# Kernel tuning notes

Hardware: AMD Instinct MI355X
Metric: run time of the kernel (lower is better)

Reference implementation:

```python
import jax, jax.numpy as jnp
import numpy as np

N_NODES = 10000
N_EDGES = 640000
IN_FEAT = 128
OUT_FEAT = 128


def setup_inputs() -> dict:
    key = jax.random.key(0)
    ks = jax.random.split(key, 12)
    inp = {
        "h": jax.random.normal(ks[0], (N_NODES, IN_FEAT), dtype=jnp.float32),
        "e": jax.random.uniform(ks[1], (N_EDGES, 1), dtype=jnp.float32),
        "src": jax.random.randint(ks[2], (N_EDGES,), 0, N_NODES, dtype=jnp.int32),
        "dst": jax.random.randint(ks[3], (N_EDGES,), 0, N_NODES, dtype=jnp.int32),
        # Linear params (torch convention: W [out, in], y = x @ W.T + b)
        "Ws_w": jax.random.normal(ks[4], (OUT_FEAT, IN_FEAT), dtype=jnp.float32) * 0.05,
        "Ws_b": jnp.zeros((OUT_FEAT,), dtype=jnp.float32),
        "Wn_w": jax.random.normal(ks[5], (OUT_FEAT, IN_FEAT), dtype=jnp.float32) * 0.05,
        "Wn_b": jnp.zeros((OUT_FEAT,), dtype=jnp.float32),
        "Wu_w": jax.random.normal(ks[6], (OUT_FEAT, IN_FEAT), dtype=jnp.float32) * 0.05,
        "Wu_b": jnp.zeros((OUT_FEAT,), dtype=jnp.float32),
        "lin_w": jax.random.normal(ks[7], (OUT_FEAT, OUT_FEAT), dtype=jnp.float32) * 0.05,
        "lin_b": jnp.zeros((OUT_FEAT,), dtype=jnp.float32),
    }
    return inp


def _mean_agg(msgs, dst, n_nodes):
    # segment-mean to destination nodes; isolated nodes (deg 0) -> 0 (DGL semantics)
    s = jax.ops.segment_sum(msgs, dst, num_segments=n_nodes)
    deg = jax.ops.segment_sum(jnp.ones((msgs.shape[0],), msgs.dtype), dst,
                              num_segments=n_nodes)
    return s / jnp.maximum(deg, 1.0)[:, None]


def reference(h, e, src, dst, Ws_w, Ws_b, Wn_w, Wn_b, Wu_w, Wu_b, lin_w, lin_b):
    n = h.shape[0]
    h_src = h[src]                      # [E, d] gather of source features
    h_p = _mean_agg(h_src * e, dst, n)  # u_mul_e + mean
    h_u = _mean_agg(h_src, dst, n)      # copy_u + mean
    h_total = (h @ Ws_w.T + Ws_b) + (h_p @ Wn_w.T + Wn_b) + (h_u @ Wu_w.T + Wu_b)
    return h_total @ lin_w.T + lin_b
```

## Files before the change

kernel.cpp:

```cpp
#include <hip/hip_runtime.h>
#include <hip/hip_bf16.h>

#define NFEAT 128
#define NPB 8
#define P 256
#define MAXN 10240
#define CAP 128
#define CVT 64

typedef __attribute__((ext_vector_type(8))) short bf16x8;
typedef __attribute__((ext_vector_type(4))) float f32x4;

__device__ __forceinline__ unsigned short f2bf(float f) {
    const unsigned int u = __float_as_uint(f);
    return (unsigned short)((u + 0x7FFFu + ((u >> 16) & 1u)) >> 16);
}
__device__ __forceinline__ float bflo(unsigned int u) {
    return __uint_as_float(u << 16);
}
__device__ __forceinline__ float bfhi(unsigned int u) {
    return __uint_as_float(u & 0xFFFF0000u);
}

__global__ __launch_bounds__(256) void hist_weights(
        const int* __restrict__ dst, unsigned char* __restrict__ hist,
        int n_edges, int n_nodes,
        const float* __restrict__ h, unsigned short* __restrict__ hb,
        const float* __restrict__ Ws, const float* __restrict__ Wn,
        const float* __restrict__ Wu,
        const float* __restrict__ Wsb, const float* __restrict__ Wnb,
        const float* __restrict__ Wub,
        const float* __restrict__ lin, const float* __restrict__ linb,
        unsigned short* __restrict__ Wcatb, float* __restrict__ btot) {
    __shared__ int lh[MAXN];
    __shared__ float cs[NFEAT], cn[NFEAT], cu[NFEAT], bsum[NFEAT];
    const int tid = threadIdx.x;
    if (blockIdx.x < P) {
        const int b = blockIdx.x;
        for (int n = tid; n < n_nodes; n += 256) lh[n] = 0;
        __syncthreads();
        const int per = (n_edges + P - 1) / P;
        const int beg = b * per;
        const int end = min(beg + per, n_edges);
        for (int i = beg + tid * 4; i < end; i += 1024) {
            if (i + 4 <= end) {
                const int4 d4 = *(const int4*)(dst + i);
                atomicAdd(&lh[d4.x], 1);
                atomicAdd(&lh[d4.y], 1);
                atomicAdd(&lh[d4.z], 1);
                atomicAdd(&lh[d4.w], 1);
            } else {
                for (int k = i; k < end; ++k) atomicAdd(&lh[dst[k]], 1);
            }
        }
        __syncthreads();
        unsigned char* hrow = hist + (size_t)b * n_nodes;
        const int n4 = n_nodes >> 2;
        for (int q = tid; q < n4; q += 256) {
            const int n = q * 4;
            const unsigned int v = (unsigned int)(lh[n] & 255)
                                 | ((unsigned int)(lh[n + 1] & 255) << 8)
                                 | ((unsigned int)(lh[n + 2] & 255) << 16)
                                 | ((unsigned int)(lh[n + 3] & 255) << 24);
            ((unsigned int*)hrow)[q] = v;
        }
        for (int n = n4 * 4 + tid; n < n_nodes; n += 256)
            hrow[n] = (unsigned char)lh[n];
    } else if (blockIdx.x < P + NFEAT) {
        const int i = blockIdx.x - P;
        const int o = tid;
        if (o < NFEAT) {
            cs[o] = Ws[o * NFEAT + i];
            cn[o] = Wn[o * NFEAT + i];
            cu[o] = Wu[o * NFEAT + i];
            bsum[o] = Wsb[o] + Wnb[o] + Wub[o];
        }
        __syncthreads();
        if (o < NFEAT) {
            float a1 = 0.f, a2 = 0.f, a3 = 0.f, ab = 0.f;
            #pragma unroll 4
            for (int k = 0; k < NFEAT; ++k) {
                const float l = lin[o * NFEAT + k];
                a1 += l * cs[k];
                a2 += l * cn[k];
                a3 += l * cu[k];
                ab += l * bsum[k];
            }
            const int tn = o >> 4, ncol = o & 15;
            const int kin = i & 31, quad = kin >> 3, j = kin & 7;
            const int tkbase = (i >> 5);
            const float av[3] = {a1, a2, a3};
            #pragma unroll
            for (int s = 0; s < 3; ++s) {
                const int tk = s * 4 + tkbase;
                const size_t idx =
                    ((size_t)(tk * 8 + tn) * 64 + quad * 16 + ncol) * 8 + j;
                Wcatb[idx] = f2bf(av[s]);
            }
            if (i == 0) btot[o] = ab + linb[o];
        }
    } else {
        const int b = blockIdx.x - P - NFEAT;
        const size_t total4 = (size_t)n_nodes * (NFEAT / 4);
        for (size_t q = (size_t)b * 256 + tid; q < total4; q += (size_t)CVT * 256) {
            const float4 v = *(const float4*)(h + q * 4);
            uint2 o;
            o.x = (unsigned int)f2bf(v.x) | ((unsigned int)f2bf(v.y) << 16);
            o.y = (unsigned int)f2bf(v.z) | ((unsigned int)f2bf(v.w) << 16);
            *(uint2*)(hb + q * 4) = o;
        }
    }
}

__global__ void col_scan(const unsigned char* __restrict__ hist,
                         unsigned char* __restrict__ base,
                         int* __restrict__ cnt, int n_nodes) {
    const int node = blockIdx.x * blockDim.x + threadIdx.x;
    if (node >= n_nodes) return;
    int run = 0;
    #pragma unroll 8
    for (int b = 0; b < P; ++b) {
        const int h = hist[(size_t)b * n_nodes + node];
        base[(size_t)b * n_nodes + node] = (unsigned char)run;
        run += h;
    }
    cnt[node] = run;
}

__global__ __launch_bounds__(256) void scatter_csr(
        const int* __restrict__ src, const int* __restrict__ dst,
        const float* __restrict__ e, const unsigned char* __restrict__ base,
        int2* __restrict__ eidx, int n_edges, int n_nodes) {
    __shared__ int lh[MAXN];
    const int tid = threadIdx.x;
    const int b = blockIdx.x;
    for (int n = tid; n < n_nodes; n += 256)
        lh[n] = n * CAP + (int)base[(size_t)b * n_nodes + n];
    __syncthreads();
    const int per = (n_edges + P - 1) / P;
    const int beg = b * per;
    const int end = min(beg + per, n_edges);
    for (int i = beg + tid * 4; i < end; i += 1024) {
        if (i + 4 <= end) {
            const int4 d4 = *(const int4*)(dst + i);
            const int4 s4 = *(const int4*)(src + i);
            const float4 e4 = *(const float4*)(e + i);
            int p0 = atomicAdd(&lh[d4.x], 1);
            int p1 = atomicAdd(&lh[d4.y], 1);
            int p2 = atomicAdd(&lh[d4.z], 1);
            int p3 = atomicAdd(&lh[d4.w], 1);
            if (p0 < (d4.x + 1) * CAP) eidx[p0] = make_int2(s4.x, __float_as_int(e4.x));
            if (p1 < (d4.y + 1) * CAP) eidx[p1] = make_int2(s4.y, __float_as_int(e4.y));
            if (p2 < (d4.z + 1) * CAP) eidx[p2] = make_int2(s4.z, __float_as_int(e4.z));
            if (p3 < (d4.w + 1) * CAP) eidx[p3] = make_int2(s4.w, __float_as_int(e4.w));
        } else {
            for (int k = i; k < end; ++k) {
                const int d = dst[k];
                const int pos = atomicAdd(&lh[d], 1);
                if (pos < (d + 1) * CAP)
                    eidx[pos] = make_int2(src[k], __float_as_int(e[k]));
            }
        }
    }
}

__global__ __launch_bounds__(256, 4) void agg_gemm(
        const float* __restrict__ h, const unsigned short* __restrict__ hb,
        const int2* __restrict__ eidx,
        const int* __restrict__ cnt, const unsigned short* __restrict__ Wcatb,
        const float* __restrict__ btot, float* __restrict__ out, int n_nodes) {
    __shared__ unsigned short Xsb[3][NPB][NFEAT];
    __shared__ int2 se[NPB][CAP];
    __shared__ int scnt[NPB];
    const int tid = threadIdx.x;
    const int n0 = blockIdx.x * NPB;

    if (tid < NPB) scnt[tid] = (n0 + tid < n_nodes) ? cnt[n0 + tid] : 0;
    __syncthreads();

    for (int i = tid; i < NPB * CAP; i += 256) {
        const int ln = i >> 7;
        const int k  = i & (CAP - 1);
        if (k < scnt[ln]) se[ln][k] = eidx[(size_t)(n0 + ln) * CAP + k];
    }
    {
        const int i = tid;
        const int n = i >> 5;
        const int c4 = i & 31;
        const int gn = n0 + n;
        float4 v = make_float4(0.f, 0.f, 0.f, 0.f);
        if (gn < n_nodes) v = *(const float4*)(h + (size_t)gn * NFEAT + c4 * 4);
        uint2 pk;
        pk.x = (unsigned int)f2bf(v.x) | ((unsigned int)f2bf(v.y) << 16);
        pk.y = (unsigned int)f2bf(v.z) | ((unsigned int)f2bf(v.w) << 16);
        *(uint2*)(&Xsb[0][n][c4 * 4]) = pk;
    }
    __syncthreads();

    {
        const int hw = tid >> 5;
        const int hl = tid & 31;
        const unsigned short* hbp = hb + hl * 4;
        const int ln = hw;
        const int n = scnt[ln];
        const int nl = min(n, CAP);
        float4 su = make_float4(0.f, 0.f, 0.f, 0.f);
        float4 sp = make_float4(0.f, 0.f, 0.f, 0.f);
        int j = 0;
        for (; j + 8 <= nl; j += 8) {
            int2 E[8];
            #pragma unroll
            for (int q = 0; q < 8; ++q) E[q] = se[ln][j + q];
            uint2 H[8];
            #pragma unroll
            for (int q = 0; q < 8; ++q)
                H[q] = *(const uint2*)(hbp + (size_t)E[q].x * NFEAT);
            #pragma unroll
            for (int q = 0; q < 8; ++q) {
                const float v = __int_as_float(E[q].y);
                const float h0 = bflo(H[q].x), h1 = bfhi(H[q].x);
                const float h2 = bflo(H[q].y), h3 = bfhi(H[q].y);
                su.x += h0; su.y += h1; su.z += h2; su.w += h3;
                sp.x += v * h0; sp.y += v * h1;
                sp.z += v * h2; sp.w += v * h3;
            }
        }
        for (; j < nl; ++j) {
            const int2 e0 = se[ln][j];
            const uint2 Hv = *(const uint2*)(hbp + (size_t)e0.x * NFEAT);
            const float v0 = __int_as_float(e0.y);
            const float h0 = bflo(Hv.x), h1 = bfhi(Hv.x);
            const float h2 = bflo(Hv.y), h3 = bfhi(Hv.y);
            su.x += h0; su.y += h1; su.z += h2; su.w += h3;
            sp.x += v0 * h0; sp.y += v0 * h1;
            sp.z += v0 * h2; sp.w += v0 * h3;
        }
        const float inv = 1.0f / fmaxf((float)n, 1.0f);
        uint2 pk;
        pk.x = (unsigned int)f2bf(sp.x * inv) | ((unsigned int)f2bf(sp.y * inv) << 16);
        pk.y = (unsigned int)f2bf(sp.z * inv) | ((unsigned int)f2bf(sp.w * inv) << 16);
        *(uint2*)(&Xsb[1][ln][hl * 4]) = pk;
        pk.x = (unsigned int)f2bf(su.x * inv) | ((unsigned int)f2bf(su.y * inv) << 16);
        pk.y = (unsigned int)f2bf(su.z * inv) | ((unsigned int)f2bf(su.w * inv) << 16);
        *(uint2*)(&Xsb[2][ln][hl * 4]) = pk;
    }
    __syncthreads();

    {
        const int wv   = tid >> 6;
        const int lane = tid & 63;
        const int mrow = lane & 15;
        const int quad = lane >> 4;
        const int tn0  = wv * 2;
        f32x4 acc0 = {0.f, 0.f, 0.f, 0.f};
        f32x4 acc1 = {0.f, 0.f, 0.f, 0.f};
        const bf16x8* Wb = (const bf16x8*)Wcatb;
        #pragma unroll
        for (int tk = 0; tk < 12; ++tk) {
            const int s  = tk >> 2;
            const int kb = (tk & 3) * 32 + quad * 8;
            const bf16x8 a  = *(const bf16x8*)(&Xsb[s][mrow & 7][kb]);
            const bf16x8 b0 = Wb[(size_t)(tk * 8 + tn0) * 64 + lane];
            const bf16x8 b1 = Wb[(size_t)(tk * 8 + tn0 + 1) * 64 + lane];
            acc0 = __builtin_amdgcn_mfma_f32_16x16x32_bf16(a, b0, acc0, 0, 0, 0);
            acc1 = __builtin_amdgcn_mfma_f32_16x16x32_bf16(a, b1, acc1, 0, 0, 0);
        }
        const int c0 = tn0 * 16 + mrow;
        const int c1 = (tn0 + 1) * 16 + mrow;
        const float bt0 = btot[c0];
        const float bt1 = btot[c1];
        #pragma unroll
        for (int r = 0; r < 4; ++r) {
            const int row = quad * 4 + r;
            const int gn = n0 + row;
            if (row < NPB && gn < n_nodes) {
                out[(size_t)gn * NFEAT + c0] = acc0[r] + bt0;
                out[(size_t)gn * NFEAT + c1] = acc1[r] + bt1;
            }
        }
    }
}

extern "C" void kernel_launch(void* const* d_in, const int* in_sizes, int n_in,
                              void* d_out, int out_size, void* d_ws, size_t ws_size,
                              hipStream_t stream) {
    const float* h     = (const float*)d_in[0];
    const float* e     = (const float*)d_in[1];
    const int*   src   = (const int*)d_in[2];
    const int*   dst   = (const int*)d_in[3];
    const float* Ws_w  = (const float*)d_in[4];
    const float* Ws_b  = (const float*)d_in[5];
    const float* Wn_w  = (const float*)d_in[6];
    const float* Wn_b  = (const float*)d_in[7];
    const float* Wu_w  = (const float*)d_in[8];
    const float* Wu_b  = (const float*)d_in[9];
    const float* lin_w = (const float*)d_in[10];
    const float* lin_b = (const float*)d_in[11];
    float* out = (float*)d_out;

    const int n_nodes = in_sizes[0] / NFEAT;
    const int n_edges = in_sizes[2];

    char* ws = (char*)d_ws;
    unsigned short* Wcatb = (unsigned short*)ws;  ws += 3 * NFEAT * NFEAT * 2;
    float* btot = (float*)ws;            ws += NFEAT * 4;
    int2*  eidx = (int2*)ws;             ws += (size_t)n_nodes * CAP * 8;
    int*   cnt  = (int*)ws;              ws += n_nodes * 4;
    unsigned short* hb = (unsigned short*)ws;  ws += (size_t)n_nodes * NFEAT * 2;
    unsigned char* hist = (unsigned char*)ws;  ws += (size_t)P * n_nodes;
    unsigned char* base = (unsigned char*)ws;  ws += (size_t)P * n_nodes;

    hist_weights<<<P + NFEAT + CVT, 256, 0, stream>>>(
        dst, hist, n_edges, n_nodes, h, hb,
        Ws_w, Wn_w, Wu_w, Ws_b, Wn_b, Wu_b, lin_w, lin_b, Wcatb, btot);

    col_scan<<<(n_nodes + 255) / 256, 256, 0, stream>>>(hist, base, cnt, n_nodes);

    scatter_csr<<<P, 256, 0, stream>>>(src, dst, e, base, eidx, n_edges, n_nodes);

    const int n_blocks = (n_nodes + NPB - 1) / NPB;
    agg_gemm<<<n_blocks, 256, 0, stream>>>(h, hb, eidx, cnt, Wcatb, btot,
                                           out, n_nodes);
}
```

Baseline: 137.2 us.

## Build per-node edge buckets with global atomics instead of histogram+scan+scatter

Replaces the three-pass deterministic bucket build (per-block shared histograms, column scan over 256 partial histograms, then scatter) with one pass that does a global atomicAdd on each node's counter and writes the edge into its fixed-capacity slot. Zeroing the counters moves into the weight/convert prep kernel, and the aggregation kernel now clamps the count to CAP when loading edges. This removes two kernel launches and the large byte-histogram traffic. In exchange it adds heavy global-atomic contention (about 64 edges per destination) and makes edge order within a bucket nondeterministic.

```diff
diff --git a/kernel.cpp b/kernel.cpp
--- a/kernel.cpp
+++ b/kernel.cpp
@@ -3,10 +3,9 @@
 
 #define NFEAT 128
 #define NPB 8
-#define P 256
-#define MAXN 10240
 #define CAP 128
 #define CVT 64
+#define SCB 640
 
 typedef __attribute__((ext_vector_type(8))) short bf16x8;
 typedef __attribute__((ext_vector_type(4))) float f32x4;
@@ -22,52 +21,23 @@
     return __uint_as_float(u & 0xFFFF0000u);
 }
 
-__global__ __launch_bounds__(256) void hist_weights(
-        const int* __restrict__ dst, unsigned char* __restrict__ hist,
-        int n_edges, int n_nodes,
+__global__ __launch_bounds__(256) void prep(
         const float* __restrict__ h, unsigned short* __restrict__ hb,
         const float* __restrict__ Ws, const float* __restrict__ Wn,
         const float* __restrict__ Wu,
         const float* __restrict__ Wsb, const float* __restrict__ Wnb,
         const float* __restrict__ Wub,
         const float* __restrict__ lin, const float* __restrict__ linb,
-        unsigned short* __restrict__ Wcatb, float* __restrict__ btot) {
-    __shared__ int lh[MAXN];
+        unsigned short* __restrict__ Wcatb, float* __restrict__ btot,
+        int* __restrict__ cnt, int n_nodes) {
     __shared__ float cs[NFEAT], cn[NFEAT], cu[NFEAT], bsum[NFEAT];
     const int tid = threadIdx.x;
-    if (blockIdx.x < P) {
-        const int b = blockIdx.x;
-        for (int n = tid; n < n_nodes; n += 256) lh[n] = 0;
-        __syncthreads();
-        const int per = (n_edges + P - 1) / P;
-        const int beg = b * per;
-        const int end = min(beg + per, n_edges);
-        for (int i = beg + tid * 4; i < end; i += 1024) {
-            if (i + 4 <= end) {
-                const int4 d4 = *(const int4*)(dst + i);
-                atomicAdd(&lh[d4.x], 1);
-                atomicAdd(&lh[d4.y], 1);
-                atomicAdd(&lh[d4.z], 1);
-                atomicAdd(&lh[d4.w], 1);
-            } else {
-                for (int k = i; k < end; ++k) atomicAdd(&lh[dst[k]], 1);
-            }
-        }
-        __syncthreads();
-        unsigned char* hrow = hist + (size_t)b * n_nodes;
-        const int n4 = n_nodes >> 2;
-        for (int q = tid; q < n4; q += 256) {
-            const int n = q * 4;
-            const unsigned int v = (unsigned int)(lh[n] & 255)
-                                 | ((unsigned int)(lh[n + 1] & 255) << 8)
-                                 | ((unsigned int)(lh[n + 2] & 255) << 16)
-                                 | ((unsigned int)(lh[n + 3] & 255) << 24);
-            ((unsigned int*)hrow)[q] = v;
-        }
-        for (int n = n4 * 4 + tid; n < n_nodes; n += 256)
-            hrow[n] = (unsigned char)lh[n];
-    } else if (blockIdx.x < P + NFEAT) {
-        const int i = blockIdx.x - P;
+    if (blockIdx.x < NFEAT) {
+        {
+            const int z = blockIdx.x * 256 + tid;
+            if (z < n_nodes) cnt[z] = 0;
+        }
+        const int i = blockIdx.x;
         const int o = tid;
         if (o < NFEAT) {
             cs[o] = Ws[o * NFEAT + i];
@@ -100,7 +70,7 @@
             if (i == 0) btot[o] = ab + linb[o];
         }
     } else {
-        const int b = blockIdx.x - P - NFEAT;
+        const int b = blockIdx.x - NFEAT;
         const size_t total4 = (size_t)n_nodes * (NFEAT / 4);
         for (size_t q = (size_t)b * 256 + tid; q < total4; q += (size_t)CVT * 256) {
             const float4 v = *(const float4*)(h + q * 4);
@@ -112,55 +82,29 @@
     }
 }
 
-__global__ void col_scan(const unsigned char* __restrict__ hist,
-                         unsigned char* __restrict__ base,
-                         int* __restrict__ cnt, int n_nodes) {
-    const int node = blockIdx.x * blockDim.x + threadIdx.x;
-    if (node >= n_nodes) return;
-    int run = 0;
-    #pragma unroll 8
-    for (int b = 0; b < P; ++b) {
-        const int h = hist[(size_t)b * n_nodes + node];
-        base[(size_t)b * n_nodes + node] = (unsigned char)run;
-        run += h;
-    }
-    cnt[node] = run;
-}
-
-__global__ __launch_bounds__(256) void scatter_csr(
+__global__ __launch_bounds__(256) void scatter_atomic(
         const int* __restrict__ src, const int* __restrict__ dst,
-        const float* __restrict__ e, const unsigned char* __restrict__ base,
-        int2* __restrict__ eidx, int n_edges, int n_nodes) {
-    __shared__ int lh[MAXN];
-    const int tid = threadIdx.x;
-    const int b = blockIdx.x;
-    for (int n = tid; n < n_nodes; n += 256)
-        lh[n] = n * CAP + (int)base[(size_t)b * n_nodes + n];
-    __syncthreads();
-    const int per = (n_edges + P - 1) / P;
-    const int beg = b * per;
-    const int end = min(beg + per, n_edges);
-    for (int i = beg + tid * 4; i < end; i += 1024) {
-        if (i + 4 <= end) {
-            const int4 d4 = *(const int4*)(dst + i);
-            const int4 s4 = *(const int4*)(src + i);
-            const float4 e4 = *(const float4*)(e + i);
-            int p0 = atomicAdd(&lh[d4.x], 1);
-            int p1 = atomicAdd(&lh[d4.y], 1);
-            int p2 = atomicAdd(&lh[d4.z], 1);
-            int p3 = atomicAdd(&lh[d4.w], 1);
-            if (p0 < (d4.x + 1) * CAP) eidx[p0] = make_int2(s4.x, __float_as_int(e4.x));
-            if (p1 < (d4.y + 1) * CAP) eidx[p1] = make_int2(s4.y, __float_as_int(e4.y));
-            if (p2 < (d4.z + 1) * CAP) eidx[p2] = make_int2(s4.z, __float_as_int(e4.z));
-            if (p3 < (d4.w + 1) * CAP) eidx[p3] = make_int2(s4.w, __float_as_int(e4.w));
-        } else {
-            for (int k = i; k < end; ++k) {
-                const int d = dst[k];
-                const int pos = atomicAdd(&lh[d], 1);
-                if (pos < (d + 1) * CAP)
-                    eidx[pos] = make_int2(src[k], __float_as_int(e[k]));
-            }
-        }
+        const float* __restrict__ e, int2* __restrict__ eidx,
+        int* __restrict__ cnt, int n_edges) {
+    const int nq = n_edges >> 2;
+    for (int q = blockIdx.x * 256 + threadIdx.x; q < nq; q += SCB * 256) {
+        const int4 d4 = ((const int4*)dst)[q];
+        const int4 s4 = ((const int4*)src)[q];
+        const float4 e4 = ((const float4*)e)[q];
+        const int p0 = atomicAdd(cnt + d4.x, 1);
+        const int p1 = atomicAdd(cnt + d4.y, 1);
+        const int p2 = atomicAdd(cnt + d4.z, 1);
+        const int p3 = atomicAdd(cnt + d4.w, 1);
+        if (p0 < CAP) eidx[(size_t)d4.x * CAP + p0] = make_int2(s4.x, __float_as_int(e4.x));
+        if (p1 < CAP) eidx[(size_t)d4.y * CAP + p1] = make_int2(s4.y, __float_as_int(e4.y));
+        if (p2 < CAP) eidx[(size_t)d4.z * CAP + p2] = make_int2(s4.z, __float_as_int(e4.z));
+        if (p3 < CAP) eidx[(size_t)d4.w * CAP + p3] = make_int2(s4.w, __float_as_int(e4.w));
+    }
+    if (blockIdx.x == 0 && threadIdx.x < (n_edges & 3)) {
+        const int i = (n_edges & ~3) + threadIdx.x;
+        const int d = dst[i];
+        const int p = atomicAdd(cnt + d, 1);
+        if (p < CAP) eidx[(size_t)d * CAP + p] = make_int2(src[i], __float_as_int(e[i]));
     }
 }
 
@@ -181,7 +125,7 @@
     for (int i = tid; i < NPB * CAP; i += 256) {
         const int ln = i >> 7;
         const int k  = i & (CAP - 1);
-        if (k < scnt[ln]) se[ln][k] = eidx[(size_t)(n0 + ln) * CAP + k];
+        if (k < min(scnt[ln], CAP)) se[ln][k] = eidx[(size_t)(n0 + ln) * CAP + k];
     }
     {
         const int i = tid;
@@ -307,16 +251,12 @@
     int2*  eidx = (int2*)ws;             ws += (size_t)n_nodes * CAP * 8;
     int*   cnt  = (int*)ws;              ws += n_nodes * 4;
     unsigned short* hb = (unsigned short*)ws;  ws += (size_t)n_nodes * NFEAT * 2;
-    unsigned char* hist = (unsigned char*)ws;  ws += (size_t)P * n_nodes;
-    unsigned char* base = (unsigned char*)ws;  ws += (size_t)P * n_nodes;
-
-    hist_weights<<<P + NFEAT + CVT, 256, 0, stream>>>(
-        dst, hist, n_edges, n_nodes, h, hb,
-        Ws_w, Wn_w, Wu_w, Ws_b, Wn_b, Wu_b, lin_w, lin_b, Wcatb, btot);
-
-    col_scan<<<(n_nodes + 255) / 256, 256, 0, stream>>>(hist, base, cnt, n_nodes);
-
-    scatter_csr<<<P, 256, 0, stream>>>(src, dst, e, base, eidx, n_edges, n_nodes);
+
+    prep<<<NFEAT + CVT, 256, 0, stream>>>(
+        h, hb, Ws_w, Wn_w, Wu_w, Ws_b, Wn_b, Wu_b, lin_w, lin_b,
+        Wcatb, btot, cnt, n_nodes);
+
+    scatter_atomic<<<SCB, 256, 0, stream>>>(src, dst, e, eidx, cnt, n_edges);
 
     const int n_blocks = (n_nodes + NPB - 1) / NPB;
     agg_gemm<<<n_blocks, 256, 0, stream>>>(h, hb, eidx, cnt, Wcatb, btot,
```

Result: slower. 150.5 us (+9.7%).

## Slice CSR scatter by destination range across XCDs, enlarge bf16 convert grid

Applied to the files above, without the earlier changes.

The scatter kernel now launches eight blocks per edge chunk. Each block owns one eighth of the destination nodes, keeps a smaller shared-memory histogram and only scatters edges that land in its slice. This is meant to raise occupancy and parallelism, and to keep each block's eidx writes inside a node range that blockIdx mapping ties to one XCD for L2 locality, at the cost of every block re-reading all edges in its chunk. CVT also grows from 64 to 384, giving more blocks to the h-to-bf16 conversion, and the agg_gemm staging loop clamps the edge count to CAP.

```diff
diff --git a/kernel.cpp b/kernel.cpp
--- a/kernel.cpp
+++ b/kernel.cpp
@@ -6,7 +6,8 @@
 #define P 256
 #define MAXN 10240
 #define CAP 128
-#define CVT 64
+#define CVT 384
+#define NXCD 8
 
 typedef __attribute__((ext_vector_type(8))) short bf16x8;
 typedef __attribute__((ext_vector_type(4))) float f32x4;
@@ -127,38 +128,59 @@
     cnt[node] = run;
 }
 
-__global__ __launch_bounds__(256) void scatter_csr(
+__global__ __launch_bounds__(256) void scatter_sliced(
         const int* __restrict__ src, const int* __restrict__ dst,
         const float* __restrict__ e, const unsigned char* __restrict__ base,
         int2* __restrict__ eidx, int n_edges, int n_nodes) {
-    __shared__ int lh[MAXN];
+    __shared__ int lh[(MAXN + NXCD - 1) / NXCD];
     const int tid = threadIdx.x;
-    const int b = blockIdx.x;
-    for (int n = tid; n < n_nodes; n += 256)
-        lh[n] = n * CAP + (int)base[(size_t)b * n_nodes + n];
+    const int r = blockIdx.x & (NXCD - 1);
+    const int s = blockIdx.x >> 3;
+    const int NPR = (n_nodes + NXCD - 1) / NXCD;
+    const int nbeg = r * NPR;
+    const int nloc = min(nbeg + NPR, n_nodes) - nbeg;
+    for (int n = tid; n < nloc; n += 256) {
+        const int g = nbeg + n;
+        lh[n] = g * CAP + (int)base[(size_t)s * n_nodes + g];
+    }
     __syncthreads();
     const int per = (n_edges + P - 1) / P;
-    const int beg = b * per;
+    const int beg = s * per;
     const int end = min(beg + per, n_edges);
     for (int i = beg + tid * 4; i < end; i += 1024) {
         if (i + 4 <= end) {
             const int4 d4 = *(const int4*)(dst + i);
             const int4 s4 = *(const int4*)(src + i);
             const float4 e4 = *(const float4*)(e + i);
-            int p0 = atomicAdd(&lh[d4.x], 1);
-            int p1 = atomicAdd(&lh[d4.y], 1);
-            int p2 = atomicAdd(&lh[d4.z], 1);
-            int p3 = atomicAdd(&lh[d4.w], 1);
-            if (p0 < (d4.x + 1) * CAP) eidx[p0] = make_int2(s4.x, __float_as_int(e4.x));
-            if (p1 < (d4.y + 1) * CAP) eidx[p1] = make_int2(s4.y, __float_as_int(e4.y));
-            if (p2 < (d4.z + 1) * CAP) eidx[p2] = make_int2(s4.z, __float_as_int(e4.z));
-            if (p3 < (d4.w + 1) * CAP) eidx[p3] = make_int2(s4.w, __float_as_int(e4.w));
+            const unsigned l0 = (unsigned)(d4.x - nbeg);
+            const unsigned l1 = (unsigned)(d4.y - nbeg);
+            const unsigned l2 = (unsigned)(d4.z - nbeg);
+            const unsigned l3 = (unsigned)(d4.w - nbeg);
+            if (l0 < (unsigned)nloc) {
+                const int p = atomicAdd(&lh[l0], 1);
+                if (p < (d4.x + 1) * CAP) eidx[p] = make_int2(s4.x, __float_as_int(e4.x));
+            }
+            if (l1 < (unsigned)nloc) {
+                const int p = atomicAdd(&lh[l1], 1);
+                if (p < (d4.y + 1) * CAP) eidx[p] = make_int2(s4.y, __float_as_int(e4.y));
+            }
+            if (l2 < (unsigned)nloc) {
+                const int p = atomicAdd(&lh[l2], 1);
+                if (p < (d4.z + 1) * CAP) eidx[p] = make_int2(s4.z, __float_as_int(e4.z));
+            }
+            if (l3 < (unsigned)nloc) {
+                const int p = atomicAdd(&lh[l3], 1);
+                if (p < (d4.w + 1) * CAP) eidx[p] = make_int2(s4.w, __float_as_int(e4.w));
+            }
         } else {
             for (int k = i; k < end; ++k) {
                 const int d = dst[k];
-                const int pos = atomicAdd(&lh[d], 1);
-                if (pos < (d + 1) * CAP)
-                    eidx[pos] = make_int2(src[k], __float_as_int(e[k]));
+                const unsigned dl = (unsigned)(d - nbeg);
+                if (dl < (unsigned)nloc) {
+                    const int pos = atomicAdd(&lh[dl], 1);
+                    if (pos < (d + 1) * CAP)
+                        eidx[pos] = make_int2(src[k], __float_as_int(e[k]));
+                }
             }
         }
     }
@@ -181,7 +203,7 @@
     for (int i = tid; i < NPB * CAP; i += 256) {
         const int ln = i >> 7;
         const int k  = i & (CAP - 1);
-        if (k < scnt[ln]) se[ln][k] = eidx[(size_t)(n0 + ln) * CAP + k];
+        if (k < min(scnt[ln], CAP)) se[ln][k] = eidx[(size_t)(n0 + ln) * CAP + k];
     }
     {
         const int i = tid;
@@ -316,7 +338,8 @@
 
     col_scan<<<(n_nodes + 255) / 256, 256, 0, stream>>>(hist, base, cnt, n_nodes);
 
-    scatter_csr<<<P, 256, 0, stream>>>(src, dst, e, base, eidx, n_edges, n_nodes);
+    scatter_sliced<<<P * NXCD, 256, 0, stream>>>(src, dst, e, base, eidx,
+                                                 n_edges, n_nodes);
 
     const int n_blocks = (n_nodes + NPB - 1) / NPB;
     agg_gemm<<<n_blocks, 256, 0, stream>>>(h, hb, eidx, cnt, Wcatb, btot,
```

New measurement: 135.4 us. Within noise of the previous version (-1.3%).
